# Kernel optimization log

Measured on AMD Instinct MI355X. Metric: run time of the kernel, lower is better.

## Reference

```python
import jax, jax.numpy as jnp
import numpy as np
from jax import lax

DIM = 384
NUM_HEADS = 6
STRIDE_Q = 1
STRIDE_KV = 2
BN_EPS = 1e-5
SCALE = DIM ** (-0.5)  # CvT scales by dim_out, not head_dim


def setup_inputs() -> dict:
    key = jax.random.key(0)
    ks = jax.random.split(key, 8)
    B, H, W, C = 32, 28, 28, DIM
    T = 1 + H * W
    x = jax.random.normal(ks[0], (B, T, C), dtype=jnp.float32)
    conv_w = jax.random.normal(ks[1], (3, C, 1, 3, 3), dtype=jnp.float32) * 0.1
    bn_gamma = jnp.ones((3, C), dtype=jnp.float32)
    bn_beta = jnp.zeros((3, C), dtype=jnp.float32)
    bn_mean = jnp.zeros((3, C), dtype=jnp.float32)
    bn_var = jnp.ones((3, C), dtype=jnp.float32)
    w_q = jax.random.normal(ks[2], (C, C), dtype=jnp.float32) * 0.02
    w_k = jax.random.normal(ks[3], (C, C), dtype=jnp.float32) * 0.02
    w_v = jax.random.normal(ks[4], (C, C), dtype=jnp.float32) * 0.02
    w_proj = jax.random.normal(ks[5], (C, C), dtype=jnp.float32) * 0.02
    b_proj = jnp.zeros((C,), dtype=jnp.float32)
    return {"x": x, "conv_w": conv_w, "bn_gamma": bn_gamma, "bn_beta": bn_beta,
            "bn_mean": bn_mean, "bn_var": bn_var, "w_q": w_q, "w_k": w_k,
            "w_v": w_v, "w_proj": w_proj, "b_proj": b_proj, "h": H, "w": W}


def _dw_conv_bn(x_sp, cw, gamma, beta, mean, var, stride):
    # x_sp: [B, C, H, W]; cw: [C, 1, 3, 3] depthwise (groups=C); inference BN
    C = x_sp.shape[1]
    y = lax.conv_general_dilated(
        x_sp, cw, window_strides=(stride, stride), padding=((1, 1), (1, 1)),
        feature_group_count=C, dimension_numbers=("NCHW", "OIHW", "NCHW"))
    inv = gamma * lax.rsqrt(var + BN_EPS)
    y = y * inv[None, :, None, None] + (beta - mean * inv)[None, :, None, None]
    B, Cc, Hc, Wc = y.shape
    return y.reshape(B, Cc, Hc * Wc).transpose(0, 2, 1)  # b (h w) c


def reference(x, conv_w, bn_gamma, bn_beta, bn_mean, bn_var,
              w_q, w_k, w_v, w_proj, b_proj, h, w):
    B, T, C = x.shape
    nh, hd = NUM_HEADS, C // NUM_HEADS
    cls_tok, x_tok = x[:, :1], x[:, 1:]
    x_sp = x_tok.reshape(B, h, w, C).transpose(0, 3, 1, 2)  # b c h w

    q = _dw_conv_bn(x_sp, conv_w[0], bn_gamma[0], bn_beta[0], bn_mean[0], bn_var[0], STRIDE_Q)
    k = _dw_conv_bn(x_sp, conv_w[1], bn_gamma[1], bn_beta[1], bn_mean[1], bn_var[1], STRIDE_KV)
    v = _dw_conv_bn(x_sp, conv_w[2], bn_gamma[2], bn_beta[2], bn_mean[2], bn_var[2], STRIDE_KV)

    q = jnp.concatenate([cls_tok, q], axis=1)
    k = jnp.concatenate([cls_tok, k], axis=1)
    v = jnp.concatenate([cls_tok, v], axis=1)

    def split_heads(t, wm):  # linear proj then b t (h d) -> b h t d
        t = t @ wm.T
        Bt, Tt, _ = t.shape
        return t.reshape(Bt, Tt, nh, hd).transpose(0, 2, 1, 3)

    q = split_heads(q, w_q)
    k = split_heads(k, w_k)
    v = split_heads(v, w_v)

    attn = jax.nn.softmax(jnp.einsum("bhld,bhtd->bhlt", q, k) * SCALE, axis=-1)
    out = jnp.einsum("bhlt,bhtd->bhld", attn, v)
    out = out.transpose(0, 2, 1, 3).reshape(B, -1, C)  # b t (h d)
    return out @ w_proj.T + b_proj
```

## Files before the change

### kernel.cpp

```cpp
#include <hip/hip_runtime.h>
#include <math.h>

#define B_SZ   32
#define C_DIM  384
#define H_IN   28
#define W_IN   28
#define TQ     785
#define TKV    197
#define NH     6
#define HD     64
#define SCALE_F 0.05103103630798287f
#define SCALE_L2E (0.05103103630798287f * 1.4426950408889634f)
#define BN_EPS_F 1e-5f

#define QROWS    25120
#define KVROWS   6304
#define QROWS_P  25216
#define KVROWS_P 6400
#define WELEM    147456
#define VT_LD    208

#define QT64     394
#define KVT64    100

typedef _Float16 f16;
typedef f16  f16x8 __attribute__((ext_vector_type(8)));
typedef f16  f16x4 __attribute__((ext_vector_type(4)));
typedef float f32x4 __attribute__((ext_vector_type(4)));

__device__ __forceinline__ void split16(float v, f16& h, f16& l) {
    h = (f16)v;
    l = (f16)(v - (float)h);
}

__device__ __forceinline__ void cp16(void* lds, const void* g) {
    __builtin_amdgcn_global_load_lds(
        (const __attribute__((address_space(1))) unsigned int*)g,
        (__attribute__((address_space(3))) unsigned int*)lds, 16, 0, 0);
}

__device__ __forceinline__ bool swz(int id, int yMax, int& y, int& n0) {
    int g = id / 24, w = id - g * 24;
    y = g * 8 + (w & 7);
    n0 = (w >> 3) * 128;
    return y < yMax;
}

__global__ __launch_bounds__(256) void prep_kernel(
    const float* __restrict__ wq, const float* __restrict__ wk,
    const float* __restrict__ wv, const float* __restrict__ wp,
    const float* __restrict__ conv_w,
    const float* __restrict__ gamma, const float* __restrict__ beta,
    const float* __restrict__ mean, const float* __restrict__ var,
    f16* __restrict__ Wh, f16* __restrict__ Wl,
    float* __restrict__ wAll)
{
    int idx = blockIdx.x * 256 + threadIdx.x;
    if (idx < 4 * WELEM) {
        int which = idx / WELEM, rem = idx - which * WELEM;
        const float* s = (which == 0) ? wq : (which == 1) ? wk : (which == 2) ? wv : wp;
        float v = s[rem];
        if (which == 0) v *= SCALE_L2E;
        f16 h, l;
        split16(v, h, l);
        Wh[idx] = h; Wl[idx] = l;
    } else if (idx < 4 * WELEM + 3 * C_DIM) {
        int k = idx - 4 * WELEM;
        int cv = k / C_DIM, c = k - cv * C_DIM;
        float inv = gamma[k] * rsqrtf(var[k] + BN_EPS_F);
#pragma unroll
        for (int t = 0; t < 9; ++t)
            wAll[cv * 3840 + t * C_DIM + c] = conv_w[(size_t)cv * C_DIM * 9 + c * 9 + t] * inv;
        wAll[cv * 3840 + 9 * C_DIM + c] = beta[k] - mean[k] * inv;
    }
}

__global__ __launch_bounds__(256) void fused_conv_kernel(
    const float* __restrict__ x,
    const float* __restrict__ wAll,
    f16* __restrict__ qh, f16* __restrict__ ql,
    f16* __restrict__ kh, f16* __restrict__ kl,
    f16* __restrict__ vh, f16* __restrict__ vl)
{
    __shared__ float sW[3 * 3840];
    int tid = threadIdx.x;
    int oi = blockIdx.x, b = blockIdx.y;

    if (oi == H_IN) {
        if (tid < 96) {
            int c = tid * 4;
            float4 v = *(const float4*)&x[(size_t)b * TQ * C_DIM + c];
            float a[4] = {v.x, v.y, v.z, v.w};
            f16x4 hv, lv;
#pragma unroll
            for (int u = 0; u < 4; ++u) { f16 h, l; split16(a[u], h, l); hv[u] = h; lv[u] = l; }
            size_t oq = (size_t)b * TQ * C_DIM + c;
            size_t okv = (size_t)b * TKV * C_DIM + c;
            *(f16x4*)&qh[oq] = hv;  *(f16x4*)&ql[oq] = lv;
            *(f16x4*)&kh[okv] = hv; *(f16x4*)&kl[okv] = lv;
            *(f16x4*)&vh[okv] = hv; *(f16x4*)&vl[okv] = lv;
        }
        return;
    }

#pragma unroll
    for (int i = 0; i < 12; ++i) {
        int idx = tid + 256 * i;
        if (idx < 2880) cp16(&sW[idx * 4], &wAll[idx * 4]);
    }
    __syncthreads();

    const size_t xb = (size_t)b * TQ * C_DIM + C_DIM;
    bool oi_even = (oi & 1) == 0;

    for (int it = 0; it < 11; ++it) {
        int idx = tid + 256 * it;
        if (idx >= 28 * 96) break;
        int oj = idx / 96, cg = idx - oj * 96;
        int c = cg * 4;

        float4 xv[9];
#pragma unroll
        for (int di = 0; di < 3; ++di) {
            int ii = oi + di - 1;
            bool rok = (ii >= 0) && (ii < H_IN);
#pragma unroll
            for (int dj = 0; dj < 3; ++dj) {
                int jj = oj + dj - 1;
                bool ok = rok && (jj >= 0) && (jj < W_IN);
                xv[di * 3 + dj] = ok ? *(const float4*)&x[xb + ((size_t)ii * W_IN + jj) * C_DIM + c]
                                     : make_float4(0.f, 0.f, 0.f, 0.f);
            }
        }

        {
            float4 acc = *(const float4*)&sW[0 * 3840 + 9 * C_DIM + c];
#pragma unroll
            for (int t = 0; t < 9; ++t) {
                float4 w4 = *(const float4*)&sW[0 * 3840 + t * C_DIM + c];
                acc.x += w4.x * xv[t].x; acc.y += w4.y * xv[t].y;
                acc.z += w4.z * xv[t].z; acc.w += w4.w * xv[t].w;
            }
            f16x4 hv, lv;
            float a[4] = {acc.x, acc.y, acc.z, acc.w};
#pragma unroll
            for (int u = 0; u < 4; ++u) { f16 h, l; split16(a[u], h, l); hv[u] = h; lv[u] = l; }
            size_t off = ((size_t)b * TQ + 1 + oi * W_IN + oj) * C_DIM + c;
            *(f16x4*)&qh[off] = hv;
            *(f16x4*)&ql[off] = lv;
        }

        if (oi_even && ((oj & 1) == 0)) {
            int p = (oi >> 1) * 14 + (oj >> 1);
            size_t off = ((size_t)b * TKV + 1 + p) * C_DIM + c;
#pragma unroll
            for (int cv = 1; cv <= 2; ++cv) {
                float4 acc = *(const float4*)&sW[cv * 3840 + 9 * C_DIM + c];
#pragma unroll
                for (int t = 0; t < 9; ++t) {
                    float4 w4 = *(const float4*)&sW[cv * 3840 + t * C_DIM + c];
                    acc.x += w4.x * xv[t].x; acc.y += w4.y * xv[t].y;
                    acc.z += w4.z * xv[t].z; acc.w += w4.w * xv[t].w;
                }
                f16x4 hv, lv;
                float a[4] = {acc.x, acc.y, acc.z, acc.w};
#pragma unroll
                for (int u = 0; u < 4; ++u) { f16 h, l; split16(a[u], h, l); hv[u] = h; lv[u] = l; }
                if (cv == 1) { *(f16x4*)&kh[off] = hv; *(f16x4*)&kl[off] = lv; }
                else         { *(f16x4*)&vh[off] = hv; *(f16x4*)&vl[off] = lv; }
            }
        }
    }
}

__device__ __forceinline__ void gemm_body(
    const f16* __restrict__ Ah, const f16* __restrict__ Al,
    const f16* __restrict__ Wh, const f16* __restrict__ Wl,
    const float* __restrict__ bias,
    float* __restrict__ Cf, f16* __restrict__ Coh, f16* __restrict__ Col,
    int M, int mode, int m0, int n0)
{
    __shared__ f16 sAh[2][64][32];
    __shared__ f16 sAl[2][64][32];
    __shared__ f16 sWh[2][128][32];
    __shared__ f16 sWl[2][128][32];

    int t = threadIdx.x;
    int wv = t >> 6, lane = t & 63;
    int wr = (wv >> 1) * 32, wc = (wv & 1) * 64;
    int lrow = lane & 15, quad = lane >> 4;
    int arow = t >> 2;
    int aseg = (t & 3) * 8;

    const f16* pAh = &Ah[(size_t)(m0 + arow) * 384 + aseg];
    const f16* pAl = &Al[(size_t)(m0 + arow) * 384 + aseg];
    const f16* pW0h = &Wh[(size_t)(n0 + arow) * 384 + aseg];
    const f16* pW1h = &Wh[(size_t)(n0 + arow + 64) * 384 + aseg];
    const f16* pW0l = &Wl[(size_t)(n0 + arow) * 384 + aseg];
    const f16* pW1l = &Wl[(size_t)(n0 + arow + 64) * 384 + aseg];

    f32x4 acc[2][4];
#pragma unroll
    for (int i = 0; i < 2; ++i)
#pragma unroll
        for (int j = 0; j < 4; ++j)
            acc[i][j] = (f32x4){0.f, 0.f, 0.f, 0.f};

    cp16(&sAh[0][arow][aseg],      pAh);
    cp16(&sAl[0][arow][aseg],      pAl);
    cp16(&sWh[0][arow][aseg],      pW0h);
    cp16(&sWh[0][arow + 64][aseg], pW1h);
    cp16(&sWl[0][arow][aseg],      pW0l);
    cp16(&sWl[0][arow + 64][aseg], pW1l);

    for (int kk = 0; kk < 12; ++kk) {
        __syncthreads();
        if (kk < 11) {
            int bn = (kk + 1) & 1;
            int ko = (kk + 1) * 32;
            cp16(&sAh[bn][arow][aseg],      pAh + ko);
            cp16(&sAl[bn][arow][aseg],      pAl + ko);
            cp16(&sWh[bn][arow][aseg],      pW0h + ko);
            cp16(&sWh[bn][arow + 64][aseg], pW1h + ko);
            cp16(&sWl[bn][arow][aseg],      pW0l + ko);
            cp16(&sWl[bn][arow + 64][aseg], pW1l + ko);
        }
        int bc = kk & 1;

        f16x8 bh[4], bl[4];
#pragma unroll
        for (int j = 0; j < 4; ++j) {
            bh[j] = *(const f16x8*)&sWh[bc][wc + j * 16 + lrow][quad * 8];
            bl[j] = *(const f16x8*)&sWl[bc][wc + j * 16 + lrow][quad * 8];
        }
#pragma unroll
        for (int i = 0; i < 2; ++i) {
            f16x8 ah = *(const f16x8*)&sAh[bc][wr + i * 16 + lrow][quad * 8];
            f16x8 al = *(const f16x8*)&sAl[bc][wr + i * 16 + lrow][quad * 8];
#pragma unroll
            for (int j = 0; j < 4; ++j) {
                acc[i][j] = __builtin_amdgcn_mfma_f32_16x16x32_f16(ah, bh[j], acc[i][j], 0, 0, 0);
                acc[i][j] = __builtin_amdgcn_mfma_f32_16x16x32_f16(ah, bl[j], acc[i][j], 0, 0, 0);
                acc[i][j] = __builtin_amdgcn_mfma_f32_16x16x32_f16(al, bh[j], acc[i][j], 0, 0, 0);
            }
        }
    }

#pragma unroll
    for (int i = 0; i < 2; ++i) {
        int grow0 = m0 + wr + i * 16 + quad * 4;
#pragma unroll
        for (int j = 0; j < 4; ++j) {
            int gcol = n0 + wc + j * 16 + lrow;
            float bb = (bias && mode == 0) ? bias[gcol] : 0.f;
#pragma unroll
            for (int r = 0; r < 4; ++r) {
                int grow = grow0 + r;
                if (grow >= M) continue;
                float v = acc[i][j][r] + bb;
                if (mode == 0) {
                    Cf[(size_t)grow * 384 + gcol] = v;
                } else if (mode == 1) {
                    f16 h, l;
                    split16(v, h, l);
                    Coh[(size_t)grow * 384 + gcol] = h;
                    Col[(size_t)grow * 384 + gcol] = l;
                } else {
                    int bb2 = grow / TKV;
                    int key = grow - bb2 * TKV;
                    size_t off = (size_t)bb2 * 384 * VT_LD + (size_t)gcol * VT_LD + key;
                    f16 h, l;
                    split16(v, h, l);
                    Coh[off] = h;
                    Col[off] = l;
                }
            }
        }
    }
}

__global__ __launch_bounds__(256) void qkv_proj_kernel(
    const f16* __restrict__ qh, const f16* __restrict__ ql,
    const f16* __restrict__ kh, const f16* __restrict__ kl,
    const f16* __restrict__ vh, const f16* __restrict__ vl,
    const f16* __restrict__ Wh, const f16* __restrict__ Wl,
    f16* __restrict__ Qph, f16* __restrict__ Qpl,
    f16* __restrict__ Kph, f16* __restrict__ Kpl,
    f16* __restrict__ VTh, f16* __restrict__ VTl,
    int yMax)
{
    int y, n0;
    if (!swz(blockIdx.x, yMax, y, n0)) return;
    if (y < QT64)
        gemm_body(qh, ql, Wh, Wl, nullptr, nullptr, Qph, Qpl, QROWS, 1, y * 64, n0);
    else if (y < QT64 + KVT64)
        gemm_body(kh, kl, Wh + WELEM, Wl + WELEM, nullptr, nullptr, Kph, Kpl,
                  KVROWS, 1, (y - QT64) * 64, n0);
    else
        gemm_body(vh, vl, Wh + 2 * WELEM, Wl + 2 * WELEM, nullptr, nullptr, VTh, VTl,
                  KVROWS, 2, (y - QT64 - KVT64) * 64, n0);
}

__global__ __launch_bounds__(256) void v_proj_kernel(
    const f16* __restrict__ vh, const f16* __restrict__ vl,
    const f16* __restrict__ Wh, const f16* __restrict__ Wl,
    f16* __restrict__ VTh, f16* __restrict__ VTl)
{
    int y, n0;
    if (!swz(blockIdx.x, KVT64, y, n0)) return;
    gemm_body(vh, vl, Wh, Wl, nullptr, nullptr, VTh, VTl, KVROWS, 2, y * 64, n0);
}

__global__ __launch_bounds__(256) void out_proj_kernel(
    const f16* __restrict__ Ah, const f16* __restrict__ Al,
    const f16* __restrict__ Wh, const f16* __restrict__ Wl,
    const float* __restrict__ bias, float* __restrict__ Cf)
{
    int y, n0;
    if (!swz(blockIdx.x, QT64, y, n0)) return;
    gemm_body(Ah, Al, Wh, Wl, bias, Cf, nullptr, nullptr, QROWS, 0, y * 64, n0);
}

__global__ __launch_bounds__(256) void attn_mfma4(
    const f16* __restrict__ Qh, const f16* __restrict__ Ql,
    const f16* __restrict__ Kh, const f16* __restrict__ Kl,
    const f16* __restrict__ VTh, const f16* __restrict__ VTl,
    f16* __restrict__ Oh, f16* __restrict__ Ol)
{
    __shared__ f16 sQh[2][64][32];
    __shared__ f16 sQl[2][64][32];
    __shared__ f16 sKh[2][64][32];
    __shared__ f16 sKl[2][64][32];
    __shared__ float sPs[64][68];

    int t = threadIdx.x;
    int wv = t >> 6, lane = t & 63;
    int c = lane & 15, quad = lane >> 4;
    int wq0 = wv * 16;
    int h = blockIdx.y, b = blockIdx.z;
    int q0 = blockIdx.x * 64;

    const size_t qbase  = (size_t)b * TQ * C_DIM + h * HD;
    const size_t kbase  = (size_t)b * TKV * C_DIM + h * HD;
    const size_t vtbase = (size_t)b * 384 * VT_LD + (size_t)h * HD * VT_LD;

#pragma unroll
    for (int i = 0; i < 2; ++i) {
        int idx = t + 256 * i;
        int ks = idx >> 8, row = (idx >> 2) & 63, sg = (idx & 3) * 8;
        cp16(&sQh[ks][row][sg], &Qh[qbase + (size_t)(q0 + row) * C_DIM + ks * 32 + sg]);
        cp16(&sQl[ks][row][sg], &Ql[qbase + (size_t)(q0 + row) * C_DIM + ks * 32 + sg]);
    }

    f32x4 s[4][4];
#pragma unroll
    for (int kt = 0; kt < 4; ++kt)
#pragma unroll
        for (int j = 0; j < 4; ++j)
            s[kt][j] = (f32x4){0.f, 0.f, 0.f, 0.f};

#pragma unroll
    for (int kt = 0; kt < 4; ++kt) {
        if (kt) __syncthreads();
#pragma unroll
        for (int i = 0; i < 2; ++i) {
            int idx = t + 256 * i;
            int ks = idx >> 8, row = (idx >> 2) & 63, sg = (idx & 3) * 8;
            cp16(&sKh[ks][row][sg], &Kh[kbase + (size_t)(kt * 64 + row) * C_DIM + ks * 32 + sg]);
            cp16(&sKl[ks][row][sg], &Kl[kbase + (size_t)(kt * 64 + row) * C_DIM + ks * 32 + sg]);
        }
        __syncthreads();

#pragma unroll
        for (int ks = 0; ks < 2; ++ks) {
            f16x8 qh8 = *(const f16x8*)&sQh[ks][wq0 + c][quad * 8];
            f16x8 ql8 = *(const f16x8*)&sQl[ks][wq0 + c][quad * 8];
#pragma unroll
            for (int j = 0; j < 4; ++j) {
                f16x8 kh8 = *(const f16x8*)&sKh[ks][j * 16 + c][quad * 8];
                f16x8 kl8 = *(const f16x8*)&sKl[ks][j * 16 + c][quad * 8];
                s[kt][j] = __builtin_amdgcn_mfma_f32_16x16x32_f16(qh8, kh8, s[kt][j], 0, 0, 0);
                s[kt][j] = __builtin_amdgcn_mfma_f32_16x16x32_f16(qh8, kl8, s[kt][j], 0, 0, 0);
                s[kt][j] = __builtin_amdgcn_mfma_f32_16x16x32_f16(ql8, kh8, s[kt][j], 0, 0, 0);
            }
        }
    }

    __syncthreads();

#pragma unroll
    for (int i = 0; i < 2; ++i) {
        int idx = t + 256 * i;
        int ks = idx >> 8, row = (idx >> 2) & 63, sg = (idx & 3) * 8;
        cp16(&sKh[ks][row][sg], &VTh[vtbase + (size_t)row * VT_LD + ks * 32 + sg]);
        cp16(&sKl[ks][row][sg], &VTl[vtbase + (size_t)row * VT_LD + ks * 32 + sg]);
    }

#pragma unroll
    for (int r = 0; r < 4; ++r) {
        s[3][0][r] = (c < 5) ? s[3][0][r] : -1e30f;
        s[3][1][r] = -1e30f;
        s[3][2][r] = -1e30f;
        s[3][3][r] = -1e30f;
    }

    float inv_r[4];
#pragma unroll
    for (int r = 0; r < 4; ++r) {
        float mx = -1e30f;
#pragma unroll
        for (int kt = 0; kt < 4; ++kt)
#pragma unroll
            for (int j = 0; j < 4; ++j)
                mx = fmaxf(mx, s[kt][j][r]);
        mx = fmaxf(mx, __shfl_xor(mx, 1));
        mx = fmaxf(mx, __shfl_xor(mx, 2));
        mx = fmaxf(mx, __shfl_xor(mx, 4));
        mx = fmaxf(mx, __shfl_xor(mx, 8));
        float sum = 0.f;
#pragma unroll
        for (int kt = 0; kt < 4; ++kt)
#pragma unroll
            for (int j = 0; j < 4; ++j) {
                float pv = exp2f(s[kt][j][r] - mx);
                s[kt][j][r] = pv;
                sum += pv;
            }
        sum += __shfl_xor(sum, 1);
        sum += __shfl_xor(sum, 2);
        sum += __shfl_xor(sum, 4);
        sum += __shfl_xor(sum, 8);
        inv_r[r] = 1.f / sum;
    }

    f32x4 o[4];
#pragma unroll
    for (int j = 0; j < 4; ++j) o[j] = (f32x4){0.f, 0.f, 0.f, 0.f};

#pragma unroll
    for (int vt = 0; vt < 4; ++vt) {
#pragma unroll
        for (int r = 0; r < 4; ++r)
#pragma unroll
            for (int j = 0; j < 4; ++j)
                sPs[wq0 + quad * 4 + r][j * 16 + c] = s[vt][j][r];

        __syncthreads();

#pragma unroll
        for (int ks = 0; ks < 2; ++ks) {
            float4 p0 = *(const float4*)&sPs[wq0 + c][ks * 32 + quad * 8];
            float4 p1 = *(const float4*)&sPs[wq0 + c][ks * 32 + quad * 8 + 4];
            float pf[8] = {p0.x, p0.y, p0.z, p0.w, p1.x, p1.y, p1.z, p1.w};
            f16x8 ph8, pl8;
#pragma unroll
            for (int ii = 0; ii < 8; ++ii) {
                f16 hh, ll;
                split16(pf[ii], hh, ll);
                ph8[ii] = hh; pl8[ii] = ll;
            }
#pragma unroll
            for (int j = 0; j < 4; ++j) {
                f16x8 vh8 = *(const f16x8*)&sKh[ks][j * 16 + c][quad * 8];
                f16x8 vl8 = *(const f16x8*)&sKl[ks][j * 16 + c][quad * 8];
                o[j] = __builtin_amdgcn_mfma_f32_16x16x32_f16(ph8, vh8, o[j], 0, 0, 0);
                o[j] = __builtin_amdgcn_mfma_f32_16x16x32_f16(ph8, vl8, o[j], 0, 0, 0);
                o[j] = __builtin_amdgcn_mfma_f32_16x16x32_f16(pl8, vh8, o[j], 0, 0, 0);
            }
        }

        if (vt < 3) {
            __syncthreads();
#pragma unroll
            for (int i = 0; i < 2; ++i) {
                int idx = t + 256 * i;
                int ks = idx >> 8, row = (idx >> 2) & 63, sg = (idx & 3) * 8;
                cp16(&sKh[ks][row][sg],
                     &VTh[vtbase + (size_t)row * VT_LD + (vt + 1) * 64 + ks * 32 + sg]);
                cp16(&sKl[ks][row][sg],
                     &VTl[vtbase + (size_t)row * VT_LD + (vt + 1) * 64 + ks * 32 + sg]);
            }
        }
    }

#pragma unroll
    for (int r = 0; r < 4; ++r) {
        int gq = q0 + wq0 + quad * 4 + r;
        if (gq >= TQ) continue;
        float inv = inv_r[r];
#pragma unroll
        for (int j = 0; j < 4; ++j) {
            float v = o[j][r] * inv;
            f16 hh, ll;
            split16(v, hh, ll);
            size_t off = (size_t)(b * TQ + gq) * C_DIM + h * HD + j * 16 + c;
            Oh[off] = hh;
            Ol[off] = ll;
        }
    }
}

extern "C" void kernel_launch(void* const* d_in, const int* in_sizes, int n_in,
                              void* d_out, int out_size, void* d_ws, size_t ws_size,
                              hipStream_t stream) {
    const float* x       = (const float*)d_in[0];
    const float* conv_w  = (const float*)d_in[1];
    const float* bn_g    = (const float*)d_in[2];
    const float* bn_b    = (const float*)d_in[3];
    const float* bn_m    = (const float*)d_in[4];
    const float* bn_v    = (const float*)d_in[5];
    const float* w_q     = (const float*)d_in[6];
    const float* w_k     = (const float*)d_in[7];
    const float* w_v     = (const float*)d_in[8];
    const float* w_proj  = (const float*)d_in[9];
    const float* b_proj  = (const float*)d_in[10];
    float* out = (float*)d_out;

    const size_t QSZ   = (size_t)QROWS_P * 384 * sizeof(f16);
    const size_t KVSZ  = (size_t)KVROWS_P * 384 * sizeof(f16);
    const size_t WSZ   = 4 * (size_t)WELEM * sizeof(f16);
    const size_t VTSZ  = (size_t)B_SZ * 384 * VT_LD * sizeof(f16);
    const size_t WALLS = 3 * 3840 * sizeof(float);

    char* p = (char*)d_ws;
    f16* qh  = (f16*)p; p += QSZ;
    f16* ql  = (f16*)p; p += QSZ;
    f16* vh  = (f16*)p; p += KVSZ;
    f16* vl  = (f16*)p; p += KVSZ;
    f16* kh  = (f16*)p; p += KVSZ;
    f16* kl  = (f16*)p; p += KVSZ;
    f16* Wh  = (f16*)p; p += WSZ;
    f16* Wl  = (f16*)p; p += WSZ;
    f16* Qph = (f16*)p; p += QSZ;
    f16* Qpl = (f16*)p; p += QSZ;
    f16* Kph = (f16*)p; p += KVSZ;
    f16* Kpl = (f16*)p; p += KVSZ;
    float* wAll = (float*)p; p += WALLS;

    size_t used = (size_t)(p - (char*)d_ws);
    bool sepVT = (ws_size >= used + 2 * VTSZ);
    f16 *VTh, *VTl;
    if (sepVT) {
        VTh = (f16*)p;
        VTl = VTh + (size_t)B_SZ * 384 * VT_LD;
    } else {
        VTh = kh;
        VTl = VTh + (size_t)B_SZ * 384 * VT_LD;
    }
    f16* oh = qh;
    f16* ol = ql;

    {
        int total = 4 * WELEM + 3 * C_DIM;
        prep_kernel<<<(total + 255) / 256, 256, 0, stream>>>(
            w_q, w_k, w_v, w_proj, conv_w, bn_g, bn_b, bn_m, bn_v, Wh, Wl, wAll);
    }

    {
        dim3 gc(H_IN + 1, B_SZ);
        fused_conv_kernel<<<gc, 256, 0, stream>>>(x, wAll, qh, ql, kh, kl, vh, vl);
    }

    if (sepVT) {
        int yMax = QT64 + 2 * KVT64;
        int nb = ((yMax + 7) / 8) * 24;
        qkv_proj_kernel<<<nb, 256, 0, stream>>>(qh, ql, kh, kl, vh, vl, Wh, Wl,
                                                Qph, Qpl, Kph, Kpl, VTh, VTl, yMax);
    } else {
        int yMax = QT64 + KVT64;
        int nb = ((yMax + 7) / 8) * 24;
        qkv_proj_kernel<<<nb, 256, 0, stream>>>(qh, ql, kh, kl, vh, vl, Wh, Wl,
                                                Qph, Qpl, Kph, Kpl, VTh, VTl, yMax);
        int nbv = ((KVT64 + 7) / 8) * 24;
        v_proj_kernel<<<nbv, 256, 0, stream>>>(vh, vl, Wh + 2 * WELEM, Wl + 2 * WELEM,
                                               VTh, VTl);
    }

    {
        dim3 ga((TQ + 63) / 64, NH, B_SZ);
        attn_mfma4<<<ga, 256, 0, stream>>>(Qph, Qpl, Kph, Kpl, VTh, VTl, oh, ol);
    }

    {
        int nb = ((QT64 + 7) / 8) * 24;
        out_proj_kernel<<<nb, 256, 0, stream>>>(oh, ol, Wh + 3 * WELEM, Wl + 3 * WELEM,
                                                b_proj, out);
    }
}
```

Measured before the change: 292.8 us.

## Enlarge projection GEMM tiles to 256x128 with triple-buffered swizzled LDS pipeline

The shared split-f16 GEMM body used by the Q/K/V and output projections moves from 64x128 tiles on 256 threads to 256x128 tiles on 512 threads, with each wave computing a 64x64 sub-tile. Global-to-LDS copies become a three-stage ring with explicit vmcnt waits, and an XOR swizzle is applied to the LDS layout to avoid bank conflicts. The MFMA block runs under raised wave priority. The aim is more operand reuse per LDS read and better hiding of load latency, at the cost of about 147 KB of LDS per block, fewer resident blocks, and more padded rows in the last M tile.

```diff
diff --git a/kernel.cpp b/kernel.cpp
--- a/kernel.cpp
+++ b/kernel.cpp
@@ -15,13 +15,13 @@
 
 #define QROWS    25120
 #define KVROWS   6304
-#define QROWS_P  25216
+#define QROWS_P  25344
 #define KVROWS_P 6400
 #define WELEM    147456
 #define VT_LD    208
 
-#define QT64     394
-#define KVT64    100
+#define QT256    99
+#define KVT256   25
 
 typedef _Float16 f16;
 typedef f16  f16x8 __attribute__((ext_vector_type(8)));
@@ -180,74 +180,90 @@
     float* __restrict__ Cf, f16* __restrict__ Coh, f16* __restrict__ Col,
     int M, int mode, int m0, int n0)
 {
-    __shared__ f16 sAh[2][64][32];
-    __shared__ f16 sAl[2][64][32];
-    __shared__ f16 sWh[2][128][32];
-    __shared__ f16 sWl[2][128][32];
-
-    int t = threadIdx.x;
-    int wv = t >> 6, lane = t & 63;
-    int wr = (wv >> 1) * 32, wc = (wv & 1) * 64;
-    int lrow = lane & 15, quad = lane >> 4;
-    int arow = t >> 2;
-    int aseg = (t & 3) * 8;
-
-    const f16* pAh = &Ah[(size_t)(m0 + arow) * 384 + aseg];
-    const f16* pAl = &Al[(size_t)(m0 + arow) * 384 + aseg];
-    const f16* pW0h = &Wh[(size_t)(n0 + arow) * 384 + aseg];
-    const f16* pW1h = &Wh[(size_t)(n0 + arow + 64) * 384 + aseg];
-    const f16* pW0l = &Wl[(size_t)(n0 + arow) * 384 + aseg];
-    const f16* pW1l = &Wl[(size_t)(n0 + arow + 64) * 384 + aseg];
-
-    f32x4 acc[2][4];
-#pragma unroll
-    for (int i = 0; i < 2; ++i)
+    __shared__ f16 lds[3 * 24576];
+
+    const int t = threadIdx.x;
+    const int wv = t >> 6, lane = t & 63;
+    const int wr = (wv >> 1) * 64;
+    const int wc = (wv & 1) * 64;
+    const int lrow = lane & 15, quad = lane >> 4;
+    const int qsw = quad ^ ((lrow >> 1) & 3);
+
+    const int sr = t >> 2;
+    const int g  = (t & 3) ^ ((t >> 3) & 3);
+
+    const f16* gA0h = Ah + (size_t)(m0 + sr) * 384 + g * 8;
+    const f16* gA1h = gA0h + 128 * 384;
+    const f16* gA0l = Al + (size_t)(m0 + sr) * 384 + g * 8;
+    const f16* gA1l = gA0l + 128 * 384;
+    const f16* gBh  = Wh + (size_t)(n0 + sr) * 384 + g * 8;
+    const f16* gBl  = Wl + (size_t)(n0 + sr) * 384 + g * 8;
+
+#define STAGE(buf, kk) do {                                   \
+        f16* d = lds + (buf) * 24576 + t * 8;                 \
+        const int ko = (kk) * 32;                             \
+        cp16(d,         gA0h + ko);                           \
+        cp16(d + 4096,  gA1h + ko);                           \
+        cp16(d + 8192,  gA0l + ko);                           \
+        cp16(d + 12288, gA1l + ko);                           \
+        cp16(d + 16384, gBh + ko);                            \
+        cp16(d + 20480, gBl + ko);                            \
+    } while (0)
+
+    f32x4 acc[4][4];
+#pragma unroll
+    for (int i = 0; i < 4; ++i)
 #pragma unroll
         for (int j = 0; j < 4; ++j)
             acc[i][j] = (f32x4){0.f, 0.f, 0.f, 0.f};
 
-    cp16(&sAh[0][arow][aseg],      pAh);
-    cp16(&sAl[0][arow][aseg],      pAl);
-    cp16(&sWh[0][arow][aseg],      pW0h);
-    cp16(&sWh[0][arow + 64][aseg], pW1h);
-    cp16(&sWl[0][arow][aseg],      pW0l);
-    cp16(&sWl[0][arow + 64][aseg], pW1l);
-
+    STAGE(0, 0);
+    STAGE(1, 1);
+
+#pragma unroll
     for (int kk = 0; kk < 12; ++kk) {
-        __syncthreads();
-        if (kk < 11) {
-            int bn = (kk + 1) & 1;
-            int ko = (kk + 1) * 32;
-            cp16(&sAh[bn][arow][aseg],      pAh + ko);
-            cp16(&sAl[bn][arow][aseg],      pAl + ko);
-            cp16(&sWh[bn][arow][aseg],      pW0h + ko);
-            cp16(&sWh[bn][arow + 64][aseg], pW1h + ko);
-            cp16(&sWl[bn][arow][aseg],      pW0l + ko);
-            cp16(&sWl[bn][arow + 64][aseg], pW1l + ko);
-        }
-        int bc = kk & 1;
-
-        f16x8 bh[4], bl[4];
+        if (kk == 11) asm volatile("s_waitcnt vmcnt(0)" ::: "memory");
+        else          asm volatile("s_waitcnt vmcnt(6)" ::: "memory");
+        __builtin_amdgcn_s_barrier();
+        __builtin_amdgcn_sched_barrier(0);
+
+        if (kk < 10) {
+            STAGE((kk + 2) % 3, kk + 2);
+            __builtin_amdgcn_sched_barrier(0);
+        }
+
+        const f16* bp = lds + (kk % 3) * 24576;
+        f16x8 ah[4], al[4], bh[4], bl[4];
+#pragma unroll
+        for (int i = 0; i < 4; ++i) {
+            int ro = (wr + i * 16 + lrow) * 32 + qsw * 8;
+            ah[i] = *(const f16x8*)&bp[ro];
+            al[i] = *(const f16x8*)&bp[8192 + ro];
+        }
 #pragma unroll
         for (int j = 0; j < 4; ++j) {
-            bh[j] = *(const f16x8*)&sWh[bc][wc + j * 16 + lrow][quad * 8];
-            bl[j] = *(const f16x8*)&sWl[bc][wc + j * 16 + lrow][quad * 8];
-        }
-#pragma unroll
-        for (int i = 0; i < 2; ++i) {
-            f16x8 ah = *(const f16x8*)&sAh[bc][wr + i * 16 + lrow][quad * 8];
-            f16x8 al = *(const f16x8*)&sAl[bc][wr + i * 16 + lrow][quad * 8];
+            int ro = (wc + j * 16 + lrow) * 32 + qsw * 8;
+            bh[j] = *(const f16x8*)&bp[16384 + ro];
+            bl[j] = *(const f16x8*)&bp[20480 + ro];
+        }
+        asm volatile("s_waitcnt lgkmcnt(0)" ::: "memory");
+        __builtin_amdgcn_sched_barrier(0);
+
+        __builtin_amdgcn_s_setprio(1);
+#pragma unroll
+        for (int i = 0; i < 4; ++i)
 #pragma unroll
             for (int j = 0; j < 4; ++j) {
-                acc[i][j] = __builtin_amdgcn_mfma_f32_16x16x32_f16(ah, bh[j], acc[i][j], 0, 0, 0);
-                acc[i][j] = __builtin_amdgcn_mfma_f32_16x16x32_f16(ah, bl[j], acc[i][j], 0, 0, 0);
-                acc[i][j] = __builtin_amdgcn_mfma_f32_16x16x32_f16(al, bh[j], acc[i][j], 0, 0, 0);
-            }
-        }
-    }
-
-#pragma unroll
-    for (int i = 0; i < 2; ++i) {
+                acc[i][j] = __builtin_amdgcn_mfma_f32_16x16x32_f16(ah[i], bh[j], acc[i][j], 0, 0, 0);
+                acc[i][j] = __builtin_amdgcn_mfma_f32_16x16x32_f16(ah[i], bl[j], acc[i][j], 0, 0, 0);
+                acc[i][j] = __builtin_amdgcn_mfma_f32_16x16x32_f16(al[i], bh[j], acc[i][j], 0, 0, 0);
+            }
+        __builtin_amdgcn_s_setprio(0);
+    }
+#undef STAGE
+
+#pragma unroll
+    for (int i = 0; i < 4; ++i) {
         int grow0 = m0 + wr + i * 16 + quad * 4;
 #pragma unroll
         for (int j = 0; j < 4; ++j) {
@@ -279,7 +295,7 @@
     }
 }
 
-__global__ __launch_bounds__(256) void qkv_proj_kernel(
+__global__ __launch_bounds__(512, 2) void qkv_proj_kernel(
     const f16* __restrict__ qh, const f16* __restrict__ ql,
     const f16* __restrict__ kh, const f16* __restrict__ kl,
     const f16* __restrict__ vh, const f16* __restrict__ vl,
@@ -291,34 +307,34 @@
 {
     int y, n0;
     if (!swz(blockIdx.x, yMax, y, n0)) return;
-    if (y < QT64)
-        gemm_body(qh, ql, Wh, Wl, nullptr, nullptr, Qph, Qpl, QROWS, 1, y * 64, n0);
-    else if (y < QT64 + KVT64)
+    if (y < QT256)
+        gemm_body(qh, ql, Wh, Wl, nullptr, nullptr, Qph, Qpl, QROWS, 1, y * 256, n0);
+    else if (y < QT256 + KVT256)
         gemm_body(kh, kl, Wh + WELEM, Wl + WELEM, nullptr, nullptr, Kph, Kpl,
-                  KVROWS, 1, (y - QT64) * 64, n0);
+                  KVROWS, 1, (y - QT256) * 256, n0);
     else
         gemm_body(vh, vl, Wh + 2 * WELEM, Wl + 2 * WELEM, nullptr, nullptr, VTh, VTl,
-                  KVROWS, 2, (y - QT64 - KVT64) * 64, n0);
-}
-
-__global__ __launch_bounds__(256) void v_proj_kernel(
+                  KVROWS, 2, (y - QT256 - KVT256) * 256, n0);
+}
+
+__global__ __launch_bounds__(512, 2) void v_proj_kernel(
     const f16* __restrict__ vh, const f16* __restrict__ vl,
     const f16* __restrict__ Wh, const f16* __restrict__ Wl,
     f16* __restrict__ VTh, f16* __restrict__ VTl)
 {
     int y, n0;
-    if (!swz(blockIdx.x, KVT64, y, n0)) return;
-    gemm_body(vh, vl, Wh, Wl, nullptr, nullptr, VTh, VTl, KVROWS, 2, y * 64, n0);
-}
-
-__global__ __launch_bounds__(256) void out_proj_kernel(
+    if (!swz(blockIdx.x, KVT256, y, n0)) return;
+    gemm_body(vh, vl, Wh, Wl, nullptr, nullptr, VTh, VTl, KVROWS, 2, y * 256, n0);
+}
+
+__global__ __launch_bounds__(512, 2) void out_proj_kernel(
     const f16* __restrict__ Ah, const f16* __restrict__ Al,
     const f16* __restrict__ Wh, const f16* __restrict__ Wl,
     const float* __restrict__ bias, float* __restrict__ Cf)
 {
     int y, n0;
-    if (!swz(blockIdx.x, QT64, y, n0)) return;
-    gemm_body(Ah, Al, Wh, Wl, bias, Cf, nullptr, nullptr, QROWS, 0, y * 64, n0);
+    if (!swz(blockIdx.x, QT256, y, n0)) return;
+    gemm_body(Ah, Al, Wh, Wl, bias, Cf, nullptr, nullptr, QROWS, 0, y * 256, n0);
 }
 
 __global__ __launch_bounds__(256) void attn_mfma4(
@@ -562,17 +578,17 @@
     }
 
     if (sepVT) {
-        int yMax = QT64 + 2 * KVT64;
+        int yMax = QT256 + 2 * KVT256;
         int nb = ((yMax + 7) / 8) * 24;
-        qkv_proj_kernel<<<nb, 256, 0, stream>>>(qh, ql, kh, kl, vh, vl, Wh, Wl,
+        qkv_proj_kernel<<<nb, 512, 0, stream>>>(qh, ql, kh, kl, vh, vl, Wh, Wl,
                                                 Qph, Qpl, Kph, Kpl, VTh, VTl, yMax);
     } else {
-        int yMax = QT64 + KVT64;
+        int yMax = QT256 + KVT256;
         int nb = ((yMax + 7) / 8) * 24;
-        qkv_proj_kernel<<<nb, 256, 0, stream>>>(qh, ql, kh, kl, vh, vl, Wh, Wl,
+        qkv_proj_kernel<<<nb, 512, 0, stream>>>(qh, ql, kh, kl, vh, vl, Wh, Wl,
                                                 Qph, Qpl, Kph, Kpl, VTh, VTl, yMax);
-        int nbv = ((KVT64 + 7) / 8) * 24;
-        v_proj_kernel<<<nbv, 256, 0, stream>>>(vh, vl, Wh + 2 * WELEM, Wl + 2 * WELEM,
+        int nbv = ((KVT256 + 7) / 8) * 24;
+        v_proj_kernel<<<nbv, 512, 0, stream>>>(vh, vl, Wh + 2 * WELEM, Wl + 2 * WELEM,
                                                VTh, VTl);
     }
 
@@ -582,8 +598,8 @@
     }
 
     {
-        int nb = ((QT64 + 7) / 8) * 24;
-        out_proj_kernel<<<nb, 256, 0, stream>>>(oh, ol, Wh + 3 * WELEM, Wl + 3 * WELEM,
+        int nb = ((QT256 + 7) / 8) * 24;
+        out_proj_kernel<<<nb, 512, 0, stream>>>(oh, ol, Wh + 3 * WELEM, Wl + 3 * WELEM,
                                                 b_proj, out);
     }
 }
```

New measurement: 303.3 us. +3.6%, slower.
